# Kernel optimization log

Measured on AMD Instinct MI355X. Metric: run time of the kernel, lower is better.

## Reference

```python
import jax, jax.numpy as jnp
import numpy as np

N = 102400   # total nodes
F = 400      # node features
E = 1638400  # edges
H = 64       # hidden channels
L = 3        # num_layers (hidden convs); +1 final conv to width 1
K = 300      # sort-pool k
NPER = 400   # nodes per graph (uniform graphs)
B = N // NPER
D = H * L + 1  # total_latent_dim = 193


def setup_inputs() -> dict:
    key = jax.random.key(0)
    ks = jax.random.split(key, 20)
    def lin(k, i, o):
        return jax.random.normal(k, (i, o), jnp.float32) / np.sqrt(i)
    inp = {
        "x": jax.random.normal(ks[0], (N, F), jnp.float32),
        "edge_index": jax.random.randint(ks[1], (2, E), 0, N, jnp.int64),
        "W1": lin(ks[2], F, H), "b1": jnp.zeros((H,), jnp.float32),
        "W2": lin(ks[3], H, H), "b2": jnp.zeros((H,), jnp.float32),
        "W3": lin(ks[4], H, H), "b3": jnp.zeros((H,), jnp.float32),
        "W4": lin(ks[5], H, 1), "b4": jnp.zeros((1,), jnp.float32),
        "cw1": jax.random.normal(ks[6], (16, 1, D), jnp.float32) / np.sqrt(D),
        "cb1": jnp.zeros((16,), jnp.float32),
        "cw2": jax.random.normal(ks[7], (32, 16, 5), jnp.float32) / np.sqrt(16 * 5),
        "cb2": jnp.zeros((32,), jnp.float32),
        "mw1": lin(ks[8], 4672, 32), "mb1": jnp.zeros((32,), jnp.float32),
        "mw2": lin(ks[9], 32, 2), "mb2": jnp.zeros((2,), jnp.float32),
    }
    return inp


def _gcn(x, W, b, src, dst, norm):
    h = x @ W                                   # [N, out]
    msg = h[src] * norm[:, None]                # [E', out]
    out = jax.ops.segment_sum(msg, dst, num_segments=N)
    return out + b


def reference(x, edge_index, W1, b1, W2, b2, W3, b3, W4, b4,
              cw1, cb1, cw2, cb2, mw1, mb1, mw2, mb2):
    # GCN normalization with self-loops (D^-1/2 (A+I) D^-1/2)
    loops = jnp.arange(N, dtype=edge_index.dtype)
    src = jnp.concatenate([edge_index[0], loops])
    dst = jnp.concatenate([edge_index[1], loops])
    deg = jax.ops.segment_sum(jnp.ones_like(src, jnp.float32), dst, num_segments=N)
    dis = jax.lax.rsqrt(jnp.maximum(deg, 1.0))
    norm = dis[src] * dis[dst]

    h1 = jnp.tanh(_gcn(x, W1, b1, src, dst, norm))
    h2 = jnp.tanh(_gcn(h1, W2, b2, src, dst, norm))
    h3 = jnp.tanh(_gcn(h2, W3, b3, src, dst, norm))
    h4 = jnp.tanh(_gcn(h3, W4, b4, src, dst, norm))
    feat = jnp.concatenate([h1, h2, h3, h4], axis=-1)  # [N, D]

    # SortAggregation: per-graph sort by last channel (descending), take top-k
    fg = feat.reshape(B, NPER, D)
    order = jnp.argsort(-fg[:, :, -1], axis=1)[:, :K]  # [B, K]
    pooled = jnp.take_along_axis(fg, order[:, :, None], axis=1)  # [B, K, D]
    z = pooled.reshape(B, 1, K * D)

    dn = ("NCH", "OIH", "NCH")
    z = jax.lax.conv_general_dilated(z, cw1, (D,), "VALID", dimension_numbers=dn)
    z = jax.nn.relu(z + cb1[None, :, None])            # [B, 16, K]
    z = jax.lax.reduce_window(z, -jnp.inf, jax.lax.max, (1, 1, 2), (1, 1, 2), "VALID")
    z = jax.lax.conv_general_dilated(z, cw2, (1,), "VALID", dimension_numbers=dn)
    z = jax.nn.relu(z + cb2[None, :, None])            # [B, 32, 146]
    z = z.reshape(B, -1)                               # [B, 4672]
    z = jax.nn.relu(z @ mw1 + mb1)
    return z @ mw2 + mb2                               # [B, 2]
```

## Files before the change

### kernel.cpp

```cpp
#include <hip/hip_runtime.h>
#include <cstdint>
#include <cstddef>

#define Nn 102400
#define Ff 400
#define Ee 1638400
#define Kk 300
#define Bb 256
#define CAP 64

__global__ void scat_k(const int* __restrict__ ei, int* __restrict__ fill,
                       int* __restrict__ csr) {
    int e = blockIdx.x * 256 + threadIdx.x;
    if (e >= Ee) return;
    int s = ei[e], d = ei[Ee + e];
    int p = atomicAdd(&fill[d], 1);
    if (p < CAP) csr[(size_t)d * CAP + p] = s;
}

__global__ __launch_bounds__(256) void sortrow_k(const int* __restrict__ deg,
                                                 int* __restrict__ csr,
                                                 double* __restrict__ dis) {
    int lane = threadIdx.x & 63;
    int v = blockIdx.x * 4 + (threadIdx.x >> 6);
    int dvf = deg[v];
    int dv = min(dvf, CAP);
    if (lane == 0) dis[v] = 1.0 / sqrt((double)(dvf + 1));
    int key = (lane < dv) ? csr[(size_t)v * CAP + lane] : 0x7FFFFFFF;
#pragma unroll
    for (int k = 2; k <= 64; k <<= 1) {
#pragma unroll
        for (int j = k >> 1; j; j >>= 1) {
            int other = __shfl_xor(key, j);
            bool up = ((lane & k) == 0);
            bool lower = ((lane & j) == 0);
            key = (lower == up) ? min(key, other) : max(key, other);
        }
    }
    if (lane < dv) csr[(size_t)v * CAP + lane] = key;
}

template <typename AT, int CH>
__global__ __launch_bounds__(128) void gemm_t84(const AT* __restrict__ A,
                                                const float* __restrict__ B,
                                                double* __restrict__ C) {
    constexpr int K = 16 * CH;
    constexpr bool F32 = (sizeof(AT) == 4);
    __shared__ __align__(16) AT As[16][64];
    __shared__ __align__(16) double Bs[16][65];
    int tid = threadIdx.x;
    int tx = tid & 15;
    int ty = tid >> 4;
    int base = blockIdx.x * 64;
    int sr = tid >> 1, sh = tid & 1;
    int bk = tid >> 3, bn = (tid & 7) * 8;
    double acc[8][4] = {};
    for (int ch = 0; ch < CH; ++ch) {
        int k0 = ch * 16;
        AT a8[8];
        const AT* ap = A + (size_t)(base + sr) * K + k0 + sh * 8;
        if constexpr (F32) {
            float4 v0 = *(const float4*)(ap);
            float4 v1 = *(const float4*)(ap + 4);
            a8[0] = v0.x; a8[1] = v0.y; a8[2] = v0.z; a8[3] = v0.w;
            a8[4] = v1.x; a8[5] = v1.y; a8[6] = v1.z; a8[7] = v1.w;
        } else {
            double2 d0 = *(const double2*)(ap);
            double2 d1 = *(const double2*)(ap + 2);
            double2 d2 = *(const double2*)(ap + 4);
            double2 d3 = *(const double2*)(ap + 6);
            a8[0] = d0.x; a8[1] = d0.y; a8[2] = d1.x; a8[3] = d1.y;
            a8[4] = d2.x; a8[5] = d2.y; a8[6] = d3.x; a8[7] = d3.y;
        }
        float4 b0 = *(const float4*)(B + (size_t)(k0 + bk) * 64 + bn);
        float4 b1 = *(const float4*)(B + (size_t)(k0 + bk) * 64 + bn + 4);
        __syncthreads();
#pragma unroll
        for (int q = 0; q < 8; ++q) As[sh * 8 + q][sr] = a8[q];
        Bs[bk][bn + 0] = (double)b0.x; Bs[bk][bn + 1] = (double)b0.y;
        Bs[bk][bn + 2] = (double)b0.z; Bs[bk][bn + 3] = (double)b0.w;
        Bs[bk][bn + 4] = (double)b1.x; Bs[bk][bn + 5] = (double)b1.y;
        Bs[bk][bn + 6] = (double)b1.z; Bs[bk][bn + 7] = (double)b1.w;
        __syncthreads();
#pragma unroll
        for (int kk = 0; kk < 16; ++kk) {
            double av[8];
            if constexpr (F32) {
                float4 f0 = *(const float4*)&As[kk][ty * 8];
                float4 f1 = *(const float4*)&As[kk][ty * 8 + 4];
                av[0] = f0.x; av[1] = f0.y; av[2] = f0.z; av[3] = f0.w;
                av[4] = f1.x; av[5] = f1.y; av[6] = f1.z; av[7] = f1.w;
            } else {
                double2 a01 = *(const double2*)&As[kk][ty * 8];
                double2 a23 = *(const double2*)&As[kk][ty * 8 + 2];
                double2 a45 = *(const double2*)&As[kk][ty * 8 + 4];
                double2 a67 = *(const double2*)&As[kk][ty * 8 + 6];
                av[0] = a01.x; av[1] = a01.y; av[2] = a23.x; av[3] = a23.y;
                av[4] = a45.x; av[5] = a45.y; av[6] = a67.x; av[7] = a67.y;
            }
            double2 b01 = *(const double2*)&Bs[kk][tx * 2];
            double2 b23 = *(const double2*)&Bs[kk][32 + tx * 2];
            double bv[4] = {b01.x, b01.y, b23.x, b23.y};
#pragma unroll
            for (int r = 0; r < 8; ++r)
#pragma unroll
                for (int c = 0; c < 4; ++c) acc[r][c] += av[r] * bv[c];
        }
    }
#pragma unroll
    for (int r = 0; r < 8; ++r) {
        double* cp = C + (size_t)(base + ty * 8 + r) * 64;
        *(double2*)(cp + tx * 2)      = make_double2(acc[r][0], acc[r][1]);
        *(double2*)(cp + 32 + tx * 2) = make_double2(acc[r][2], acc[r][3]);
    }
}

__global__ __launch_bounds__(256) void agg64_k(const double* __restrict__ t,
                                               const float* __restrict__ bias,
                                               const double* __restrict__ dis,
                                               const int* __restrict__ deg,
                                               const int* __restrict__ csr,
                                               double* __restrict__ out,
                                               const float* __restrict__ W4,
                                               double* __restrict__ t4) {
    int lane = threadIdx.x & 63;
    int wv = __builtin_amdgcn_readfirstlane(threadIdx.x >> 6);
    int v = blockIdx.x * 4 + wv;
    int dv = min(deg[v], CAP);
    double dsv = dis[v];
    const int* row = csr + (size_t)v * CAP;
    double acc = 0.0;
    int j = 0;
    for (; j + 8 <= dv; j += 8) {
        int u[8]; double d[8], tv[8];
#pragma unroll
        for (int q = 0; q < 8; ++q) u[q] = row[j + q];
#pragma unroll
        for (int q = 0; q < 8; ++q) tv[q] = t[(size_t)u[q] * 64 + lane];
#pragma unroll
        for (int q = 0; q < 8; ++q) d[q] = dis[u[q]];
#pragma unroll
        for (int q = 0; q < 8; ++q) acc += d[q] * tv[q];
    }
    for (; j < dv; ++j) {
        int u = row[j];
        acc += dis[u] * t[(size_t)u * 64 + lane];
    }
    acc += dsv * t[(size_t)v * 64 + lane];
    double res = tanh((double)bias[lane] + dsv * acc);
    out[(size_t)v * 64 + lane] = res;
    if (t4 != nullptr) {
        double x = res * (double)W4[lane];
#pragma unroll
        for (int o = 32; o > 0; o >>= 1) x += __shfl_xor(x, o);
        if (lane == 0) t4[v] = x;
    }
}

__global__ void agg1_k(const double* __restrict__ t4, const double* __restrict__ dis,
                       const int* __restrict__ deg, const int* __restrict__ csr,
                       const float* __restrict__ b4, double* __restrict__ h4) {
    int v = blockIdx.x * 256 + threadIdx.x;
    if (v >= Nn) return;
    int dv = min(deg[v], CAP);
    double dsv = dis[v];
    double acc = 0.0;
    const int* row = csr + (size_t)v * CAP;
    for (int j = 0; j < dv; ++j) { int u = row[j]; acc += dis[u] * t4[u]; }
    acc += dsv * t4[v];
    h4[v] = tanh((double)b4[0] + dsv * acc);
}

__global__ __launch_bounds__(512) void sort_k(const double* __restrict__ h4,
                                              int* __restrict__ order) {
    __shared__ unsigned long long kv[512];
    __shared__ int ki[512];
    int tid = threadIdx.x, g = blockIdx.x;
    unsigned long long key = ~0ull;
    if (tid < 400) {
        unsigned long long u = (unsigned long long)__double_as_longlong(h4[g * 400 + tid]);
        u = (u & 0x8000000000000000ull) ? ~u : (u | 0x8000000000000000ull);
        key = ~u;
    }
    kv[tid] = key; ki[tid] = tid;
    __syncthreads();
    for (int size = 2; size <= 512; size <<= 1) {
        for (int stride = size >> 1; stride > 0; stride >>= 1) {
            int p = tid ^ stride;
            if (p > tid) {
                bool asc = ((tid & size) == 0);
                unsigned long long a = kv[tid], b = kv[p];
                int ia = ki[tid], ib = ki[p];
                bool gt = (a > b) || (a == b && ia > ib);
                if (gt == asc) { kv[tid] = b; kv[p] = a; ki[tid] = ib; ki[p] = ia; }
            }
            __syncthreads();
        }
    }
    if (tid < Kk) order[g * Kk + tid] = ki[tid];
}

__global__ __launch_bounds__(128) void conv1_k(const double* __restrict__ h1,
                                               const double* __restrict__ h2,
                                               const double* __restrict__ h3,
                                               const double* __restrict__ h4,
                                               const int* __restrict__ order,
                                               const float* __restrict__ cw1,
                                               const float* __restrict__ cb1,
                                               float* __restrict__ z1) {
    __shared__ double wt[193 * 16];
    int tid = threadIdx.x, b = blockIdx.y;
    for (int i = tid; i < 193 * 16; i += 128) {
        int c = i / 193, d = i % 193;
        wt[d * 16 + c] = (double)cw1[i];
    }
    __syncthreads();
    int kpos = blockIdx.x * 128 + tid;
    if (kpos >= Kk) return;
    int n = b * 400 + order[b * Kk + kpos];
    double acc[16];
#pragma unroll
    for (int c = 0; c < 16; ++c) acc[c] = (double)cb1[c];
    const double* bases[3] = {h1 + (size_t)n * 64, h2 + (size_t)n * 64, h3 + (size_t)n * 64};
    for (int r = 0; r < 3; ++r) {
        const double* p = bases[r];
        for (int d = 0; d < 64; ++d) {
            double xv = p[d];
            const double* wp = &wt[((size_t)r * 64 + d) * 16];
#pragma unroll
            for (int c = 0; c < 16; ++c) acc[c] += xv * wp[c];
        }
    }
    double xl = h4[n];
    {
        const double* wp = &wt[192 * 16];
#pragma unroll
        for (int c = 0; c < 16; ++c) acc[c] += xl * wp[c];
    }
#pragma unroll
    for (int c = 0; c < 16; ++c)
        z1[((size_t)b * 16 + c) * 300 + kpos] = (float)fmax(acc[c], 0.0);
}

__global__ __launch_bounds__(256) void tail_k(const float* __restrict__ z1,
                                              const float* __restrict__ cw2,
                                              const float* __restrict__ cb2,
                                              const float* __restrict__ mw1,
                                              const float* __restrict__ mb1,
                                              const float* __restrict__ mw2,
                                              const float* __restrict__ mb2,
                                              float* __restrict__ out) {
    __shared__ float lz[16 * 150];
    __shared__ float lw[2560];
    __shared__ float lz3[4672];
    __shared__ double red[256];
    __shared__ double s4[32];
    int b = blockIdx.x, tid = threadIdx.x;
    for (int i = tid; i < 2400; i += 256) {
        int bc = i / 150, j = i % 150;
        const float* zp = z1 + ((size_t)b * 16 + bc) * 300 + 2 * j;
        lz[i] = fmaxf(zp[0], zp[1]);
    }
    for (int i = tid; i < 2560; i += 256) lw[i] = cw2[i];
    __syncthreads();
    for (int o = tid; o < 4672; o += 256) {
        int co = o / 146, j = o % 146;
        float acc = cb2[co];
#pragma unroll
        for (int ci = 0; ci < 16; ++ci)
#pragma unroll
            for (int tt = 0; tt < 5; ++tt)
                acc += lz[ci * 150 + j + tt] * lw[co * 80 + ci * 5 + tt];
        lz3[o] = fmaxf(acc, 0.f);
    }
    __syncthreads();
    int o = tid & 31, part = tid >> 5;
    double acc = 0.0;
    for (int i = part * 584; i < (part + 1) * 584; ++i)
        acc += (double)lz3[i] * (double)mw1[(size_t)i * 32 + o];
    red[tid] = acc;
    __syncthreads();
    if (tid < 32) {
        double s = 0.0;
#pragma unroll
        for (int p = 0; p < 8; ++p) s += red[p * 32 + tid];
        s4[tid] = fmax(s + (double)mb1[tid], 0.0);
    }
    __syncthreads();
    if (tid < 2) {
        double s = (double)mb2[tid];
#pragma unroll
        for (int j = 0; j < 32; ++j) s += s4[j] * (double)mw2[j * 2 + tid];
        out[b * 2 + tid] = (float)s;
    }
}

extern "C" void kernel_launch(void* const* d_in, const int* in_sizes, int n_in,
                              void* d_out, int out_size, void* d_ws, size_t ws_size,
                              hipStream_t stream) {
    const float* x   = (const float*)d_in[0];
    const int*   ei  = (const int*)d_in[1];
    const float* W1  = (const float*)d_in[2];  const float* b1  = (const float*)d_in[3];
    const float* W2  = (const float*)d_in[4];  const float* b2  = (const float*)d_in[5];
    const float* W3  = (const float*)d_in[6];  const float* b3  = (const float*)d_in[7];
    const float* W4  = (const float*)d_in[8];  const float* b4  = (const float*)d_in[9];
    const float* cw1 = (const float*)d_in[10]; const float* cb1 = (const float*)d_in[11];
    const float* cw2 = (const float*)d_in[12]; const float* cb2 = (const float*)d_in[13];
    const float* mw1 = (const float*)d_in[14]; const float* mb1 = (const float*)d_in[15];
    const float* mw2 = (const float*)d_in[16]; const float* mb2 = (const float*)d_in[17];
    float* out = (float*)d_out;

    const size_t N64 = (size_t)Nn * 64;
    double* t   = (double*)d_ws;
    double* h1  = t + N64;
    double* h2  = h1 + N64;
    double* h3  = h2 + N64;
    double* t4  = h3 + N64;
    double* h4  = t4 + Nn;
    double* dis = h4 + Nn;
    int*   fill = (int*)(dis + Nn);
    int*   csr  = fill + Nn;
    int*   order = csr + (size_t)Nn * CAP;
    float* z1 = (float*)t;

    hipMemsetAsync(fill, 0, sizeof(int) * (size_t)Nn, stream);

    scat_k<<<Ee / 256, 256, 0, stream>>>(ei, fill, csr);
    sortrow_k<<<Nn / 4, 256, 0, stream>>>(fill, csr, dis);

    gemm_t84<float, 25> <<<Nn / 64, 128, 0, stream>>>(x, W1, t);
    agg64_k<<<Nn / 4, 256, 0, stream>>>(t, b1, dis, fill, csr, h1, nullptr, nullptr);
    gemm_t84<double, 4><<<Nn / 64, 128, 0, stream>>>(h1, W2, t);
    agg64_k<<<Nn / 4, 256, 0, stream>>>(t, b2, dis, fill, csr, h2, nullptr, nullptr);
    gemm_t84<double, 4><<<Nn / 64, 128, 0, stream>>>(h2, W3, t);
    agg64_k<<<Nn / 4, 256, 0, stream>>>(t, b3, dis, fill, csr, h3, W4, t4);

    agg1_k<<<Nn / 256, 256, 0, stream>>>(t4, dis, fill, csr, b4, h4);

    sort_k<<<Bb, 512, 0, stream>>>(h4, order);
    conv1_k<<<dim3(3, Bb), 128, 0, stream>>>(h1, h2, h3, h4, order, cw1, cb1, z1);
    tail_k<<<Bb, 256, 0, stream>>>(z1, cw2, cb2, mw1, mb1, mw2, mb2, out);
}
```

Baseline: 1.093 ms.

## Shrink GEMM tiles to one wave and widen aggregation gather batching

The dense transform GEMM now runs one 64-thread wave per block, covering 32 rows instead of 64, with a padded shared A tile for the double-precision path. Each thread loads 16 B values instead of 8. The aggregation kernel batches 16 neighbor gathers at a time with a 4-wide fallback loop, and makes neighbor indices wave-uniform via readfirstlane so they can be scalar loads. The aim is more blocks for occupancy and more memory-level parallelism in the gathers, at the cost of less tile reuse per block and higher register pressure.

```diff
diff --git a/kernel.cpp b/kernel.cpp
--- a/kernel.cpp
+++ b/kernel.cpp
@@ -41,19 +41,20 @@
 }
 
 template <typename AT, int CH>
-__global__ __launch_bounds__(128) void gemm_t84(const AT* __restrict__ A,
-                                                const float* __restrict__ B,
-                                                double* __restrict__ C) {
+__global__ __launch_bounds__(64) void gemm_w32(const AT* __restrict__ A,
+                                               const float* __restrict__ B,
+                                               double* __restrict__ C) {
     constexpr int K = 16 * CH;
     constexpr bool F32 = (sizeof(AT) == 4);
-    __shared__ __align__(16) AT As[16][64];
+    constexpr int APD = F32 ? 32 : 33;
+    __shared__ __align__(16) AT As[16 * APD];
     __shared__ __align__(16) double Bs[16][65];
     int tid = threadIdx.x;
     int tx = tid & 15;
     int ty = tid >> 4;
-    int base = blockIdx.x * 64;
+    int base = blockIdx.x * 32;
     int sr = tid >> 1, sh = tid & 1;
-    int bk = tid >> 3, bn = (tid & 7) * 8;
+    int bk = tid >> 2, bn = (tid & 3) * 16;
     double acc[8][4] = {};
     for (int ch = 0; ch < CH; ++ch) {
         int k0 = ch * 16;
@@ -72,29 +73,34 @@
             a8[0] = d0.x; a8[1] = d0.y; a8[2] = d1.x; a8[3] = d1.y;
             a8[4] = d2.x; a8[5] = d2.y; a8[6] = d3.x; a8[7] = d3.y;
         }
-        float4 b0 = *(const float4*)(B + (size_t)(k0 + bk) * 64 + bn);
-        float4 b1 = *(const float4*)(B + (size_t)(k0 + bk) * 64 + bn + 4);
+        float4 bv4[4];
+        const float* bp = B + (size_t)(k0 + bk) * 64 + bn;
+#pragma unroll
+        for (int q = 0; q < 4; ++q) bv4[q] = *(const float4*)(bp + q * 4);
         __syncthreads();
 #pragma unroll
-        for (int q = 0; q < 8; ++q) As[sh * 8 + q][sr] = a8[q];
-        Bs[bk][bn + 0] = (double)b0.x; Bs[bk][bn + 1] = (double)b0.y;
-        Bs[bk][bn + 2] = (double)b0.z; Bs[bk][bn + 3] = (double)b0.w;
-        Bs[bk][bn + 4] = (double)b1.x; Bs[bk][bn + 5] = (double)b1.y;
-        Bs[bk][bn + 6] = (double)b1.z; Bs[bk][bn + 7] = (double)b1.w;
+        for (int q = 0; q < 8; ++q) As[(sh * 8 + q) * APD + sr] = a8[q];
+#pragma unroll
+        for (int q = 0; q < 4; ++q) {
+            Bs[bk][bn + q * 4 + 0] = (double)bv4[q].x;
+            Bs[bk][bn + q * 4 + 1] = (double)bv4[q].y;
+            Bs[bk][bn + q * 4 + 2] = (double)bv4[q].z;
+            Bs[bk][bn + q * 4 + 3] = (double)bv4[q].w;
+        }
         __syncthreads();
 #pragma unroll
         for (int kk = 0; kk < 16; ++kk) {
             double av[8];
             if constexpr (F32) {
-                float4 f0 = *(const float4*)&As[kk][ty * 8];
-                float4 f1 = *(const float4*)&As[kk][ty * 8 + 4];
+                float4 f0 = *(const float4*)&As[kk * APD + ty * 8];
+                float4 f1 = *(const float4*)&As[kk * APD + ty * 8 + 4];
                 av[0] = f0.x; av[1] = f0.y; av[2] = f0.z; av[3] = f0.w;
                 av[4] = f1.x; av[5] = f1.y; av[6] = f1.z; av[7] = f1.w;
             } else {
-                double2 a01 = *(const double2*)&As[kk][ty * 8];
-                double2 a23 = *(const double2*)&As[kk][ty * 8 + 2];
-                double2 a45 = *(const double2*)&As[kk][ty * 8 + 4];
-                double2 a67 = *(const double2*)&As[kk][ty * 8 + 6];
+                double2 a01 = *(const double2*)&As[kk * APD + ty * 8];
+                double2 a23 = *(const double2*)&As[kk * APD + ty * 8 + 2];
+                double2 a45 = *(const double2*)&As[kk * APD + ty * 8 + 4];
+                double2 a67 = *(const double2*)&As[kk * APD + ty * 8 + 6];
                 av[0] = a01.x; av[1] = a01.y; av[2] = a23.x; av[3] = a23.y;
                 av[4] = a45.x; av[5] = a45.y; av[6] = a67.x; av[7] = a67.y;
             }
@@ -131,19 +137,30 @@
     const int* row = csr + (size_t)v * CAP;
     double acc = 0.0;
     int j = 0;
-    for (; j + 8 <= dv; j += 8) {
-        int u[8]; double d[8], tv[8];
-#pragma unroll
-        for (int q = 0; q < 8; ++q) u[q] = row[j + q];
-#pragma unroll
-        for (int q = 0; q < 8; ++q) tv[q] = t[(size_t)u[q] * 64 + lane];
-#pragma unroll
-        for (int q = 0; q < 8; ++q) d[q] = dis[u[q]];
-#pragma unroll
-        for (int q = 0; q < 8; ++q) acc += d[q] * tv[q];
+    for (; j + 16 <= dv; j += 16) {
+        int u[16]; double d[16], tv[16];
+#pragma unroll
+        for (int q = 0; q < 16; ++q) u[q] = __builtin_amdgcn_readfirstlane(row[j + q]);
+#pragma unroll
+        for (int q = 0; q < 16; ++q) tv[q] = t[(size_t)u[q] * 64 + lane];
+#pragma unroll
+        for (int q = 0; q < 16; ++q) d[q] = dis[u[q]];
+#pragma unroll
+        for (int q = 0; q < 16; ++q) acc += d[q] * tv[q];
+    }
+    for (; j + 4 <= dv; j += 4) {
+        int u[4]; double d[4], tv[4];
+#pragma unroll
+        for (int q = 0; q < 4; ++q) u[q] = __builtin_amdgcn_readfirstlane(row[j + q]);
+#pragma unroll
+        for (int q = 0; q < 4; ++q) tv[q] = t[(size_t)u[q] * 64 + lane];
+#pragma unroll
+        for (int q = 0; q < 4; ++q) d[q] = dis[u[q]];
+#pragma unroll
+        for (int q = 0; q < 4; ++q) acc += d[q] * tv[q];
     }
     for (; j < dv; ++j) {
-        int u = row[j];
+        int u = __builtin_amdgcn_readfirstlane(row[j]);
         acc += dis[u] * t[(size_t)u * 64 + lane];
     }
     acc += dsv * t[(size_t)v * 64 + lane];
@@ -328,11 +345,11 @@
     scat_k<<<Ee / 256, 256, 0, stream>>>(ei, fill, csr);
     sortrow_k<<<Nn / 4, 256, 0, stream>>>(fill, csr, dis);
 
-    gemm_t84<float, 25> <<<Nn / 64, 128, 0, stream>>>(x, W1, t);
+    gemm_w32<float, 25> <<<Nn / 32, 64, 0, stream>>>(x, W1, t);
     agg64_k<<<Nn / 4, 256, 0, stream>>>(t, b1, dis, fill, csr, h1, nullptr, nullptr);
-    gemm_t84<double, 4><<<Nn / 64, 128, 0, stream>>>(h1, W2, t);
+    gemm_w32<double, 4><<<Nn / 32, 64, 0, stream>>>(h1, W2, t);
     agg64_k<<<Nn / 4, 256, 0, stream>>>(t, b2, dis, fill, csr, h2, nullptr, nullptr);
-    gemm_t84<double, 4><<<Nn / 64, 128, 0, stream>>>(h2, W3, t);
+    gemm_w32<double, 4><<<Nn / 32, 64, 0, stream>>>(h2, W3, t);
     agg64_k<<<Nn / 4, 256, 0, stream>>>(t, b3, dis, fill, csr, h3, W4, t4);
 
     agg1_k<<<Nn / 256, 256, 0, stream>>>(t4, dis, fill, csr, b4, h4);
```

New measurement: 1.093 ms. Within noise of the previous version (-0.0%).
